# Optimization experiments

Measured on AMD Instinct MI355X. Metric: run time of the kernel, lower is better.

Reference implementation:

```python
import jax, jax.numpy as jnp
import numpy as np

IN_F = 256
OUT_F = 64
ALPHA = 0.2  # LeakyReLU negative slope
MASK_VAL = -9e15


def _glorot(key, shape):
    r = np.sqrt(6.0 / (shape[0] + shape[1]))
    return jax.random.uniform(key, shape, jnp.float32, -r, r)


def setup_inputs() -> dict:
    key = jax.random.key(0)
    k_h, k_adj, k_W, k_a = jax.random.split(key, 4)
    B, N = 4, 4096
    h = jax.random.normal(k_h, (B, N, IN_F), jnp.float32)
    adj = jax.random.randint(k_adj, (B, N, N), 0, 2, jnp.int32)
    W = _glorot(k_W, (IN_F, OUT_F))
    a = _glorot(k_a, (2 * OUT_F, 1))
    bias = jnp.zeros((OUT_F,), jnp.float32)
    return {"h": h, "adj": adj, "W": W, "a": a, "bias": bias}


def reference(h, adj, W, a, bias):
    # Wh: [B, N, F_out]
    Wh = jnp.matmul(h, W) + bias
    # additive attention: e_ij = leakyrelu(Wh_i . a1 + Wh_j . a2)
    Wh1 = jnp.matmul(Wh, a[:OUT_F, :])   # [B, N, 1]
    Wh2 = jnp.matmul(Wh, a[OUT_F:, :])   # [B, N, 1]
    e = Wh1 + jnp.swapaxes(Wh2, 2, 1)    # [B, N, N]
    e = jnp.where(e > 0, e, ALPHA * e)   # LeakyReLU
    e = jnp.where(adj > 0, e, MASK_VAL)
    attention = jax.nn.softmax(e, axis=2)
    h_prime = jnp.matmul(attention, Wh)  # [B, N, F_out]
    return jax.nn.elu(h_prime)           # concat=True -> ELU
```

## Files before the change

kernel.cpp:

```cpp
#include <hip/hip_runtime.h>
#include <hip/hip_bf16.h>
#include <cstdint>

#define IN_F 256
#define OUT_F 64
#define NB 4
#define NN 4096
#define ALPHA 0.2f

typedef __attribute__((ext_vector_type(4))) float f32x4;
typedef __attribute__((ext_vector_type(4))) int i32x4;
typedef __attribute__((ext_vector_type(8))) short bf16x8;

static __device__ __forceinline__ ushort f2bf(float x) {
  uint32_t u = __float_as_uint(x);
  uint32_t r = (u + 0x7fffu + ((u >> 16) & 1u)) >> 16;
  return (ushort)r;
}

static __device__ __forceinline__ void gl16(const void* g, void* l) {
  __builtin_amdgcn_global_load_lds(
      (const __attribute__((address_space(1))) void*)g,
      (__attribute__((address_space(3))) void*)l, 16, 0, 0);
}

#define K1_ROWS 64
__global__ __launch_bounds__(256) void k1_gemm(
    const float* __restrict__ h, const float* __restrict__ W,
    const float* __restrict__ a, const float* __restrict__ bias,
    ushort* __restrict__ WhT, float* __restrict__ Wh1, float* __restrict__ Wh2)
{
  __shared__ float hs[K1_ROWS][33];
  __shared__ float Ws[32][64];
  const int t  = threadIdx.x;
  const int tx = t & 15;
  const int ty = t >> 4;
  const int row0 = blockIdx.x * K1_ROWS;

  float acc[4][4] = {};

  for (int k0 = 0; k0 < IN_F; k0 += 32) {
    #pragma unroll
    for (int s = 0; s < 2; ++s) {
      int f4 = t + 256 * s;
      int r = f4 >> 3, c4 = f4 & 7;
      f32x4 v = *(const f32x4*)(h + (size_t)(row0 + r) * IN_F + k0 + c4 * 4);
      *(f32x4*)&hs[r][c4 * 4] = v;
    }
    #pragma unroll
    for (int s = 0; s < 2; ++s) {
      int f4 = t + 256 * s;
      int kk = f4 >> 4, c4 = f4 & 15;
      *(f32x4*)&Ws[kk][c4 * 4] = *(const f32x4*)(W + (size_t)(k0 + kk) * OUT_F + c4 * 4);
    }
    __syncthreads();
    #pragma unroll 8
    for (int kk = 0; kk < 32; ++kk) {
      f32x4 bv = *(const f32x4*)&Ws[kk][tx * 4];
      #pragma unroll
      for (int i = 0; i < 4; ++i) {
        float av = hs[ty * 4 + i][kk];
        acc[i][0] += av * bv[0];
        acc[i][1] += av * bv[1];
        acc[i][2] += av * bv[2];
        acc[i][3] += av * bv[3];
      }
    }
    __syncthreads();
  }

  #pragma unroll
  for (int i = 0; i < 4; ++i) {
    int row = row0 + ty * 4 + i;
    float s1 = 0.f, s2 = 0.f;
    #pragma unroll
    for (int j = 0; j < 4; ++j) {
      float v = acc[i][j] + bias[tx * 4 + j];
      acc[i][j] = v;
      s1 += v * a[tx * 4 + j];
      s2 += v * a[64 + tx * 4 + j];
    }
    #pragma unroll
    for (int off = 1; off < 16; off <<= 1) {
      s1 += __shfl_xor(s1, off);
      s2 += __shfl_xor(s2, off);
    }
    if (tx == 0) { Wh1[row] = s1; Wh2[row] = s2; }
    int bb = row >> 12;
    int n  = row & 4095;
    #pragma unroll
    for (int j = 0; j < 4; ++j) {
      WhT[(((size_t)(bb * OUT_F + tx * 4 + j)) << 12) + n] = f2bf(acc[i][j]);
    }
  }
}

__global__ __launch_bounds__(256) void k1b_max(const float* __restrict__ Wh2,
                                               float* __restrict__ M2)
{
  const int b = blockIdx.x;
  float m = -3.0e38f;
  for (int i = threadIdx.x; i < NN; i += 256) m = fmaxf(m, Wh2[(b << 12) + i]);
  #pragma unroll
  for (int off = 1; off < 64; off <<= 1) m = fmaxf(m, __shfl_xor(m, off));
  __shared__ float sm[4];
  if ((threadIdx.x & 63) == 0) sm[threadIdx.x >> 6] = m;
  __syncthreads();
  if (threadIdx.x == 0) M2[b] = fmaxf(fmaxf(sm[0], sm[1]), fmaxf(sm[2], sm[3]));
}

__global__ __launch_bounds__(256) void k2_attn(
    const int* __restrict__ adj, const ushort* __restrict__ WhT,
    const float* __restrict__ Wh1, const float* __restrict__ Wh2,
    const float* __restrict__ M2, float* __restrict__ out)
{
  __shared__ char smem[65536];
  const int t  = threadIdx.x;
  const int l  = t & 63;
  const int w  = t >> 6;
  const int rh = w >> 1;
  const int kq = w & 1;
  const int g  = l >> 4;
  const int lr = l & 15;
  const int b  = blockIdx.y;
  const int r0 = blockIdx.x << 5;

  const float LOG2E = 1.4426950408889634f;
  const float wh1 = Wh1[(b << 12) + r0 + rh * 16 + lr];
  float mr = wh1 + M2[b];
  mr = mr > 0.f ? mr : ALPHA * mr;
  const float nm2 = -mr * LOG2E;

  const int srow = t >> 4;
  const int scol = ((t & 15) << 4) ^ ((srow & 15) << 4);
  const int* adjsrc0 = adj + ((size_t)b << 24) + ((size_t)(r0 + srow) << 12) + (scol >> 2);
  const int* adjsrc1 = adjsrc0 + ((size_t)16 << 12);
  const int wfeat = t >> 3;
  const int wcolb = ((t & 7) << 4) ^ ((wfeat & 7) << 4);
  const ushort* whtsrc0 = WhT + ((size_t)(b * OUT_F + wfeat) << 12) + (wcolb >> 1);
  const ushort* whtsrc1 = whtsrc0 + ((size_t)32 << 12);
  const int la0 = t << 4;
  const int la1 = 4096 + (t << 4);

  auto STAGE = [&](int s, int bsel) {
    const size_t jo = (size_t)s << 6;
    char* ba = smem + (bsel << 14);
    gl16(adjsrc0 + jo, ba + la0);
    gl16(adjsrc1 + jo, ba + la1);
    gl16(whtsrc0 + jo, ba + 8192 + la0);
    gl16(whtsrc1 + jo, ba + 8192 + la1);
  };

  f32x4 a0 = {0.f,0.f,0.f,0.f}, a1 = {0.f,0.f,0.f,0.f};
  f32x4 a2 = {0.f,0.f,0.f,0.f}, a3 = {0.f,0.f,0.f,0.f};
  f32x4 as = {0.f,0.f,0.f,0.f};
  bf16x8 ones;
  #pragma unroll
  for (int i = 0; i < 8; ++i) ones[i] = (short)0x3F80;

  const int rowloc = rh * 16 + lr;
  const int xa   = kq * 128 + g * 32;
  const int sa   = (rowloc & 15) << 4;
  const int innw = (kq * 64 + g * 16) ^ ((lr & 7) << 4);

  auto COMPUTE = [&](int s, int bsel) {
    const char* bufA = smem + (bsel << 14);
    const char* bufW = bufA + 8192;
    const char* w2b  = smem + 49152 + (s << 8) + kq * 128 + g * 32;
    i32x4 ad0 = *(const i32x4*)(bufA + rowloc * 256 + ((xa +  0) ^ sa));
    i32x4 ad1 = *(const i32x4*)(bufA + rowloc * 256 + ((xa + 16) ^ sa));
    f32x4 w20 = *(const f32x4*)(w2b);
    f32x4 w21 = *(const f32x4*)(w2b + 16);
    bf16x8 b0 = *(const bf16x8*)(bufW + (lr      ) * 128 + innw);
    bf16x8 b1 = *(const bf16x8*)(bufW + (lr + 16 ) * 128 + innw);
    bf16x8 b2 = *(const bf16x8*)(bufW + (lr + 32 ) * 128 + innw);
    bf16x8 b3 = *(const bf16x8*)(bufW + (lr + 48 ) * 128 + innw);

    float p[8];
    #pragma unroll
    for (int i = 0; i < 8; ++i) {
      float w2 = (i < 4) ? w20[i] : w21[i - 4];
      int   am = (i < 4) ? ad0[i] : ad1[i - 4];
      float s_ = wh1 + w2;
      float lk = fmaf(ALPHA, fminf(s_, 0.f), fmaxf(s_, 0.f));
      float pe = exp2f(fmaf(lk, LOG2E, nm2));
      p[i] = (am > 0) ? pe : 0.0f;
    }
    union { bf16x8 v; uint32_t u[4]; } af;
    #pragma unroll
    for (int i = 0; i < 4; ++i)
      asm("v_cvt_pk_bf16_f32 %0, %1, %2" : "=v"(af.u[i]) : "v"(p[2*i]), "v"(p[2*i+1]));

    as = __builtin_amdgcn_mfma_f32_16x16x32_bf16(af.v, ones, as, 0, 0, 0);
    a0 = __builtin_amdgcn_mfma_f32_16x16x32_bf16(af.v, b0,   a0, 0, 0, 0);
    a1 = __builtin_amdgcn_mfma_f32_16x16x32_bf16(af.v, b1,   a1, 0, 0, 0);
    a2 = __builtin_amdgcn_mfma_f32_16x16x32_bf16(af.v, b2,   a2, 0, 0, 0);
    a3 = __builtin_amdgcn_mfma_f32_16x16x32_bf16(af.v, b3,   a3, 0, 0, 0);
  };

  {
    const float* w2src = Wh2 + (b << 12) + (t << 2);
    #pragma unroll
    for (int i = 0; i < 4; ++i)
      gl16(w2src + (i << 10), smem + 49152 + (i << 12) + (t << 4));
  }
  STAGE(0, 0);
  STAGE(1, 1);

  int bs = 0, bs2 = 2;
  for (int s = 0; s < 63; ++s) {
    asm volatile("s_waitcnt vmcnt(4)" ::: "memory");
    __builtin_amdgcn_s_barrier();
    COMPUTE(s, bs);
    if (s < 62) STAGE(s + 2, bs2);
    bs  = (bs  == 2) ? 0 : bs  + 1;
    bs2 = (bs2 == 2) ? 0 : bs2 + 1;
  }
  asm volatile("s_waitcnt vmcnt(0)" ::: "memory");
  __builtin_amdgcn_s_barrier();
  COMPUTE(63, bs);

  __syncthreads();
  float* sacc = (float*)smem;
  float* ssum = (float*)(smem + 17408);
  #pragma unroll
  for (int r = 0; r < 4; ++r) {
    int rr = g * 4 + r;
    float* dst = sacc + (w * 16 + rr) * 68;
    dst[ 0 + lr] = a0[r];
    dst[16 + lr] = a1[r];
    dst[32 + lr] = a2[r];
    dst[48 + lr] = a3[r];
    if (lr == 0) ssum[w * 16 + rr] = as[r];
  }
  __syncthreads();

  const int row = t >> 3;
  const int c0  = (t & 7) << 3;
  const int rh2 = row >> 4, r16 = row & 15;
  const float* p0 = sacc + ((rh2 * 2 + 0) * 16 + r16) * 68;
  const float* p1 = sacc + ((rh2 * 2 + 1) * 16 + r16) * 68;
  float d = ssum[(rh2 * 2 + 0) * 16 + r16] + ssum[(rh2 * 2 + 1) * 16 + r16];
  float inv = 1.0f / d;
  f32x4 o0, o1;
  #pragma unroll
  for (int j = 0; j < 4; ++j) {
    float x = (p0[c0 + j] + p1[c0 + j]) * inv;
    o0[j] = x > 0.f ? x : expm1f(x);
    float y = (p0[c0 + 4 + j] + p1[c0 + 4 + j]) * inv;
    o1[j] = y > 0.f ? y : expm1f(y);
  }
  size_t ob = ((size_t)((b << 12) + r0 + row) << 6) + c0;
  *(f32x4*)(out + ob)     = o0;
  *(f32x4*)(out + ob + 4) = o1;
}

extern "C" void kernel_launch(void* const* d_in, const int* in_sizes, int n_in,
                              void* d_out, int out_size, void* d_ws, size_t ws_size,
                              hipStream_t stream) {
  const float* h    = (const float*)d_in[0];
  const int*   adj  = (const int*)d_in[1];
  const float* W    = (const float*)d_in[2];
  const float* a    = (const float*)d_in[3];
  const float* bias = (const float*)d_in[4];
  float* out = (float*)d_out;

  char* ws = (char*)d_ws;
  ushort* WhT = (ushort*)ws;
  float*  Wh1 = (float*)(ws + (size_t)NB * OUT_F * NN * 2);
  float*  Wh2 = Wh1 + NB * NN;
  float*  M2  = Wh2 + NB * NN;

  k1_gemm<<<dim3(NB * NN / K1_ROWS), 256, 0, stream>>>(h, W, a, bias, WhT, Wh1, Wh2);
  k1b_max<<<dim3(NB), 256, 0, stream>>>(Wh2, M2);
  k2_attn<<<dim3(NN / 32, NB), 256, 0, stream>>>(adj, WhT, Wh1, Wh2, M2, out);
}
```

Measured before the change: 91.31 us.

## Enlarge attention tile to 64 rows with 512 threads, shrink projection tile

The attention kernel now handles 64 rows per block with 8 waves and 512 threads, using 90 KB of dynamic LDS. Each staged WhT tile is reused by twice as many rows, which halves the WhT global traffic per output row, and the triple-buffer indexing is simplified to s%3. The projection GEMM now processes 32 rows per block instead of 64, doubling the grid for better occupancy. In exchange, the larger LDS footprint limits how many attention blocks fit per CU, and the attention grid shrinks to 256 blocks.

```diff
diff --git a/kernel.cpp b/kernel.cpp
--- a/kernel.cpp
+++ b/kernel.cpp
@@ -24,28 +24,25 @@
       (__attribute__((address_space(3))) void*)l, 16, 0, 0);
 }
 
-#define K1_ROWS 64
 __global__ __launch_bounds__(256) void k1_gemm(
     const float* __restrict__ h, const float* __restrict__ W,
     const float* __restrict__ a, const float* __restrict__ bias,
     ushort* __restrict__ WhT, float* __restrict__ Wh1, float* __restrict__ Wh2)
 {
-  __shared__ float hs[K1_ROWS][33];
+  __shared__ float hs[32][33];
   __shared__ float Ws[32][64];
   const int t  = threadIdx.x;
   const int tx = t & 15;
   const int ty = t >> 4;
-  const int row0 = blockIdx.x * K1_ROWS;
-
-  float acc[4][4] = {};
+  const int row0 = blockIdx.x * 32;
+
+  float acc[2][4] = {};
 
   for (int k0 = 0; k0 < IN_F; k0 += 32) {
-    #pragma unroll
-    for (int s = 0; s < 2; ++s) {
-      int f4 = t + 256 * s;
-      int r = f4 >> 3, c4 = f4 & 7;
-      f32x4 v = *(const f32x4*)(h + (size_t)(row0 + r) * IN_F + k0 + c4 * 4);
-      *(f32x4*)&hs[r][c4 * 4] = v;
+    {
+      int r = t >> 3, c4 = t & 7;
+      *(f32x4*)&hs[r][c4 * 4] =
+          *(const f32x4*)(h + (size_t)(row0 + r) * IN_F + k0 + c4 * 4);
     }
     #pragma unroll
     for (int s = 0; s < 2; ++s) {
@@ -57,21 +54,20 @@
     #pragma unroll 8
     for (int kk = 0; kk < 32; ++kk) {
       f32x4 bv = *(const f32x4*)&Ws[kk][tx * 4];
+      float av0 = hs[ty * 2 + 0][kk];
+      float av1 = hs[ty * 2 + 1][kk];
       #pragma unroll
-      for (int i = 0; i < 4; ++i) {
-        float av = hs[ty * 4 + i][kk];
-        acc[i][0] += av * bv[0];
-        acc[i][1] += av * bv[1];
-        acc[i][2] += av * bv[2];
-        acc[i][3] += av * bv[3];
+      for (int j = 0; j < 4; ++j) {
+        acc[0][j] += av0 * bv[j];
+        acc[1][j] += av1 * bv[j];
       }
     }
     __syncthreads();
   }
 
   #pragma unroll
-  for (int i = 0; i < 4; ++i) {
-    int row = row0 + ty * 4 + i;
+  for (int i = 0; i < 2; ++i) {
+    int row = row0 + ty * 2 + i;
     float s1 = 0.f, s2 = 0.f;
     #pragma unroll
     for (int j = 0; j < 4; ++j) {
@@ -109,46 +105,47 @@
   if (threadIdx.x == 0) M2[b] = fmaxf(fmaxf(sm[0], sm[1]), fmaxf(sm[2], sm[3]));
 }
 
-__global__ __launch_bounds__(256) void k2_attn(
+#define BUFSZ 24576
+#define WH2_OFF 73728
+__global__ __launch_bounds__(512) void k2_attn(
     const int* __restrict__ adj, const ushort* __restrict__ WhT,
     const float* __restrict__ Wh1, const float* __restrict__ Wh2,
     const float* __restrict__ M2, float* __restrict__ out)
 {
-  __shared__ char smem[65536];
+  extern __shared__ char smem[];
   const int t  = threadIdx.x;
   const int l  = t & 63;
   const int w  = t >> 6;
-  const int rh = w >> 1;
+  const int rq = w >> 1;
   const int kq = w & 1;
   const int g  = l >> 4;
   const int lr = l & 15;
   const int b  = blockIdx.y;
-  const int r0 = blockIdx.x << 5;
+  const int r0 = blockIdx.x << 6;
 
   const float LOG2E = 1.4426950408889634f;
-  const float wh1 = Wh1[(b << 12) + r0 + rh * 16 + lr];
+  const int   rowl  = rq * 16 + lr;
+  const float wh1 = Wh1[(b << 12) + r0 + rowl];
   float mr = wh1 + M2[b];
   mr = mr > 0.f ? mr : ALPHA * mr;
   const float nm2 = -mr * LOG2E;
-
-  const int srow = t >> 4;
-  const int scol = ((t & 15) << 4) ^ ((srow & 15) << 4);
-  const int* adjsrc0 = adj + ((size_t)b << 24) + ((size_t)(r0 + srow) << 12) + (scol >> 2);
-  const int* adjsrc1 = adjsrc0 + ((size_t)16 << 12);
-  const int wfeat = t >> 3;
-  const int wcolb = ((t & 7) << 4) ^ ((wfeat & 7) << 4);
-  const ushort* whtsrc0 = WhT + ((size_t)(b * OUT_F + wfeat) << 12) + (wcolb >> 1);
-  const ushort* whtsrc1 = whtsrc0 + ((size_t)32 << 12);
-  const int la0 = t << 4;
-  const int la1 = 4096 + (t << 4);
-
-  auto STAGE = [&](int s, int bsel) {
-    const size_t jo = (size_t)s << 6;
-    char* ba = smem + (bsel << 14);
-    gl16(adjsrc0 + jo, ba + la0);
-    gl16(adjsrc1 + jo, ba + la1);
-    gl16(whtsrc0 + jo, ba + 8192 + la0);
-    gl16(whtsrc1 + jo, ba + 8192 + la1);
+  asm volatile("" :: "v"(nm2), "v"(wh1));
+
+  const int*    adjb = adj + ((size_t)b << 24) + ((size_t)r0 << 12);
+  const ushort* whb  = WhT + ((size_t)(b * OUT_F) << 12);
+  const int rowA = t >> 4,           mlA = (t & 15) ^ (rowA & 7);
+  const int rowB = (t + 512) >> 4,   mlB = (t & 15) ^ (rowB & 7);
+  const int fW   = t >> 3,           mlW = (t & 7) ^ (fW & 7);
+  const int*    srcA = adjb + (size_t)rowA * 4096 + mlA * 4;
+  const int*    srcB = adjb + (size_t)rowB * 4096 + mlB * 4;
+  const ushort* srcW = whb + ((size_t)fW << 12) + mlW * 8;
+  const int ldsA = t << 4, ldsB = (t + 512) << 4, ldsW = 16384 + (t << 4);
+
+  auto STAGE = [&](int s) {
+    char* base = smem + (s % 3) * BUFSZ;
+    gl16(srcA + s * 64, base + ldsA);
+    gl16(srcB + s * 64, base + ldsB);
+    gl16(srcW + s * 64, base + ldsW);
   };
 
   f32x4 a0 = {0.f,0.f,0.f,0.f}, a1 = {0.f,0.f,0.f,0.f};
@@ -158,23 +155,24 @@
   #pragma unroll
   for (int i = 0; i < 8; ++i) ones[i] = (short)0x3F80;
 
-  const int rowloc = rh * 16 + lr;
-  const int xa   = kq * 128 + g * 32;
-  const int sa   = (rowloc & 15) << 4;
-  const int innw = (kq * 64 + g * 16) ^ ((lr & 7) << 4);
-
-  auto COMPUTE = [&](int s, int bsel) {
-    const char* bufA = smem + (bsel << 14);
-    const char* bufW = bufA + 8192;
-    const char* w2b  = smem + 49152 + (s << 8) + kq * 128 + g * 32;
-    i32x4 ad0 = *(const i32x4*)(bufA + rowloc * 256 + ((xa +  0) ^ sa));
-    i32x4 ad1 = *(const i32x4*)(bufA + rowloc * 256 + ((xa + 16) ^ sa));
+  const int swzA = (rowl & 7) << 4;
+  const int swzW = (lr & 7) << 4;
+  const int offA0 = (kq * 128 + g * 32) ^ swzA;
+  const int offA1 = (kq * 128 + g * 32 + 16) ^ swzA;
+  const int offW  = (kq * 64 + g * 16) ^ swzW;
+
+  auto COMPUTE = [&](int s) {
+    const char* base = smem + (s % 3) * BUFSZ;
+    i32x4 ad0 = *(const i32x4*)(base + rowl * 256 + offA0);
+    i32x4 ad1 = *(const i32x4*)(base + rowl * 256 + offA1);
+    const char* wb = base + 16384;
+    bf16x8 b0 = *(const bf16x8*)(wb + (lr     ) * 128 + offW);
+    bf16x8 b1 = *(const bf16x8*)(wb + (lr + 16) * 128 + offW);
+    bf16x8 b2 = *(const bf16x8*)(wb + (lr + 32) * 128 + offW);
+    bf16x8 b3 = *(const bf16x8*)(wb + (lr + 48) * 128 + offW);
+    const char* w2b = smem + WH2_OFF + (s << 8) + kq * 128 + g * 32;
     f32x4 w20 = *(const f32x4*)(w2b);
     f32x4 w21 = *(const f32x4*)(w2b + 16);
-    bf16x8 b0 = *(const bf16x8*)(bufW + (lr      ) * 128 + innw);
-    bf16x8 b1 = *(const bf16x8*)(bufW + (lr + 16 ) * 128 + innw);
-    bf16x8 b2 = *(const bf16x8*)(bufW + (lr + 32 ) * 128 + innw);
-    bf16x8 b3 = *(const bf16x8*)(bufW + (lr + 48 ) * 128 + innw);
 
     float p[8];
     #pragma unroll
@@ -199,48 +197,42 @@
   };
 
   {
-    const float* w2src = Wh2 + (b << 12) + (t << 2);
-    #pragma unroll
-    for (int i = 0; i < 4; ++i)
-      gl16(w2src + (i << 10), smem + 49152 + (i << 12) + (t << 4));
-  }
-  STAGE(0, 0);
-  STAGE(1, 1);
-
-  int bs = 0, bs2 = 2;
-  for (int s = 0; s < 63; ++s) {
-    asm volatile("s_waitcnt vmcnt(4)" ::: "memory");
+    const float* w2src = Wh2 + (b << 12);
+    gl16(w2src + (t << 2),         smem + WH2_OFF + (t << 4));
+    gl16(w2src + ((t + 512) << 2), smem + WH2_OFF + ((t + 512) << 4));
+  }
+  STAGE(0);
+  STAGE(1);
+
+  for (int s = 0; s < 64; ++s) {
+    if (s < 63) asm volatile("s_waitcnt vmcnt(3)" ::: "memory");
+    else        asm volatile("s_waitcnt vmcnt(0)" ::: "memory");
     __builtin_amdgcn_s_barrier();
-    COMPUTE(s, bs);
-    if (s < 62) STAGE(s + 2, bs2);
-    bs  = (bs  == 2) ? 0 : bs  + 1;
-    bs2 = (bs2 == 2) ? 0 : bs2 + 1;
-  }
-  asm volatile("s_waitcnt vmcnt(0)" ::: "memory");
-  __builtin_amdgcn_s_barrier();
-  COMPUTE(63, bs);
+    asm volatile("" ::: "memory");
+    COMPUTE(s);
+    if (s < 62) STAGE(s + 2);
+  }
 
   __syncthreads();
   float* sacc = (float*)smem;
-  float* ssum = (float*)(smem + 17408);
+  float* ssum = (float*)(smem + 34816);
   #pragma unroll
   for (int r = 0; r < 4; ++r) {
-    int rr = g * 4 + r;
-    float* dst = sacc + (w * 16 + rr) * 68;
+    int rr = rq * 16 + g * 4 + r;
+    float* dst = sacc + (kq * 64 + rr) * 68;
     dst[ 0 + lr] = a0[r];
     dst[16 + lr] = a1[r];
     dst[32 + lr] = a2[r];
     dst[48 + lr] = a3[r];
-    if (lr == 0) ssum[w * 16 + rr] = as[r];
+    if (lr == 0) ssum[kq * 64 + rr] = as[r];
   }
   __syncthreads();
 
   const int row = t >> 3;
   const int c0  = (t & 7) << 3;
-  const int rh2 = row >> 4, r16 = row & 15;
-  const float* p0 = sacc + ((rh2 * 2 + 0) * 16 + r16) * 68;
-  const float* p1 = sacc + ((rh2 * 2 + 1) * 16 + r16) * 68;
-  float d = ssum[(rh2 * 2 + 0) * 16 + r16] + ssum[(rh2 * 2 + 1) * 16 + r16];
+  const float* p0 = sacc + row * 68;
+  const float* p1 = sacc + (64 + row) * 68;
+  float d = ssum[row] + ssum[64 + row];
   float inv = 1.0f / d;
   f32x4 o0, o1;
   #pragma unroll
@@ -271,7 +263,7 @@
   float*  Wh2 = Wh1 + NB * NN;
   float*  M2  = Wh2 + NB * NN;
 
-  k1_gemm<<<dim3(NB * NN / K1_ROWS), 256, 0, stream>>>(h, W, a, bias, WhT, Wh1, Wh2);
+  k1_gemm<<<dim3(NB * NN / 32), 256, 0, stream>>>(h, W, a, bias, WhT, Wh1, Wh2);
   k1b_max<<<dim3(NB), 256, 0, stream>>>(Wh2, M2);
-  k2_attn<<<dim3(NN / 32, NB), 256, 0, stream>>>(adj, WhT, Wh1, Wh2, M2, out);
-}
+  k2_attn<<<dim3(NN / 64, NB), 512, 90112, stream>>>(adj, WhT, Wh1, Wh2, M2, out);
+}
```

Result: faster. 78.16 us (-14.4%).
